# Performance work log

Hardware: AMD Instinct MI355X
Metric: run time of the kernel (lower is better)

## Reference

```python
import jax, jax.numpy as jnp
import numpy as np

# Module dims (match init_kwargs / input_specs)
V = 25        # number of graph nodes (chain skeleton)
K = 3         # max receptive-field size (neighbors incl. self), padded
CIN = 64
COUT = 64
N = 16
T = 512
TK = 3        # temporal_kernel
PAD = TK // 2 # time_pad default


def _build_graph():
    # Chain adjacency with self-links: node i <-> {i-1, i, i+1}
    A = np.zeros((V, V), np.float32)
    for i in range(V):
        A[i, i] = 1.0
        if i > 0:
            A[i, i - 1] = 1.0
        if i < V - 1:
            A[i, i + 1] = 1.0
    # Pad each node's neighbor list to K entries; mask marks real neighbors.
    idx = np.zeros((V, K), np.int32)
    mask = np.zeros((V, K), bool)
    for i in range(V):
        nb = np.where(A[i] != 0)[0]
        idx[i, : len(nb)] = nb
        mask[i, : len(nb)] = True
    return idx, mask


def setup_inputs() -> dict:
    key = jax.random.key(0)
    k_x, k_w, k_b = jax.random.split(key, 3)
    x = jax.random.normal(k_x, (N, CIN, V, T), dtype=jnp.float32)
    # One Conv2d kernel per node: [V, C_out, C_in, K, TK]; padded neighbor
    # slots are zeroed via mask inside reference().
    W = jax.random.normal(k_w, (V, COUT, CIN, K, TK), dtype=jnp.float32) * 0.05
    b = jax.random.normal(k_b, (V, COUT), dtype=jnp.float32) * 0.05
    idx_np, mask_np = _build_graph()
    return {
        "x": x,
        "W": W,
        "b": b,
        "idx": jnp.asarray(idx_np),
        "mask": jnp.asarray(mask_np),
    }


def reference(x, W, b, idx, mask):
    # x: [N, C, V, T]; W: [V, O, C, K, TK]; b: [V, O]; idx/mask: [V, K]
    Tt = x.shape[-1]
    # Zero out padded neighbor slots so padded rows contribute nothing
    # (equivalent to torch's variable-height per-node kernels).
    Wm = jnp.where(mask[:, None, None, :, None], W, 0.0)
    # Temporal zero padding (Conv2d padding=(0, time_pad))
    xp = jnp.pad(x, ((0, 0), (0, 0), (0, 0), (PAD, PAD)))
    # Batched neighbor gather: [N, C, V, K, T + 2*PAD]
    g = xp[:, :, idx, :]
    # Cross-correlation over the TK temporal taps (stride 1)
    out = jnp.zeros((x.shape[0], W.shape[1], V, Tt), dtype=x.dtype)
    for kt in range(TK):
        out = out + jnp.einsum(
            "ncvkt,vock->novt", g[..., kt : kt + Tt], Wm[..., kt]
        )
    out = out + b.T[None, :, :, None]  # per-node bias [O, V]
    return out
```

## Files before the change

kernel.cpp:

```cpp
#include <hip/hip_runtime.h>
#include <hip/hip_bf16.h>

#define NB   16
#define CINC 64
#define COUTC 64
#define NV   25
#define TLEN 512
#define KK   3
#define TKK  3

typedef short short8 __attribute__((ext_vector_type(8)));
typedef float f32x4  __attribute__((ext_vector_type(4)));
typedef float f32x16 __attribute__((ext_vector_type(16)));

#define XT_ROWS 514
#define XS_BYTES 16640
#define NWT3BLK (NV * 9)

__device__ __forceinline__ unsigned pack_bf16(float lo, float hi) {
  __hip_bfloat16 l = __float2bfloat16(lo);
  __hip_bfloat16 h = __float2bfloat16(hi);
  unsigned short ul = *reinterpret_cast<unsigned short*>(&l);
  unsigned short uh = *reinterpret_cast<unsigned short*>(&h);
  return (unsigned)ul | ((unsigned)uh << 16);
}

__global__ __launch_bounds__(256) void prep_all(
    const float* __restrict__ x, const float* __restrict__ W,
    const unsigned char* __restrict__ mask_raw,
    __hip_bfloat16* __restrict__ Wt3, __hip_bfloat16* __restrict__ xT) {
  __shared__ float ts[64][65];
  int bid = blockIdx.x;
  if (bid < NWT3BLK) {
    int blk = bid;
    int v = blk / 9, kkt = blk % 9, k = kkt / 3, kt = kkt % 3;
    const int* mi = (const int*)mask_raw;
    int ok = 1;
    for (int i = 0; i < 18; ++i) {
      int m = mi[i];
      if (m != 0 && m != 1) ok = 0;
    }
    int m = ok ? mi[v * KK + k] : (int)(mask_raw[v * KK + k] != 0);
    const float* Wv = W + (size_t)v * COUTC * CINC * 9;
    __hip_bfloat16* dst = Wt3 + (size_t)blk * 4096;
    for (int i = threadIdx.x; i < 4096; i += 256) {
      int e     = i & 7;
      int lane  = (i >> 3) & 63;
      int ks    = (i >> 9) & 3;
      int oslab = i >> 11;
      int o = oslab * 32 + (lane & 31);
      int c = ks * 16 + 8 * (lane >> 5) + e;
      float val = m ? Wv[(o * CINC + c) * 9 + k * 3 + kt] : 0.f;
      dst[i] = __float2bfloat16(val);
    }
    return;
  }
  bid -= NWT3BLK;
  const int tb = (bid & 7) * 64;
  const int vn = bid >> 3;
  const int v  = vn % NV;
  const int n  = vn / NV;
  const int tid = threadIdx.x;
  for (int i = tid; i < 1024; i += 256) {
    int c = i >> 4, tq = (i & 15) * 4;
    float4 val = *(const float4*)(x + (((size_t)n * CINC + c) * NV + v) * TLEN + tb + tq);
    ts[c][tq + 0] = val.x;
    ts[c][tq + 1] = val.y;
    ts[c][tq + 2] = val.z;
    ts[c][tq + 3] = val.w;
  }
  __syncthreads();
  unsigned* base = (unsigned*)(xT + ((size_t)(n * NV + v) * XT_ROWS) * CINC);
  for (int i = tid; i < 2048; i += 256) {
    int c2 = i & 31, t = i >> 5;
    base[(tb + 1 + t) * 32 + c2] = pack_bf16(ts[2 * c2][t], ts[2 * c2 + 1][t]);
  }
  if (tb == 0 && tid < 32) base[tid] = 0u;
  if (tb == TLEN - 64 && tid < 32) base[513 * 32 + tid] = 0u;
}

__device__ __forceinline__ const char* slab_base(const __hip_bfloat16* xT,
                                                 int n, int vk, int tb) {
  return (const char*)xT + ((size_t)(n * NV + vk) * XT_ROWS + tb) * 128;
}

__global__ __launch_bounds__(256) void lcn_mfma32(
    const __hip_bfloat16* __restrict__ xT,
    const __hip_bfloat16* __restrict__ Wt3,
    const float* __restrict__ bias,
    const int* __restrict__ idx,
    float* __restrict__ out) {
  __shared__ char xs[KK][XS_BYTES];

  const int tb   = blockIdx.x * 128;
  const int n    = blockIdx.y;
  const int v    = blockIdx.z;
  const int tid  = threadIdx.x;
  const int lane = tid & 63;
  const int wave = tid >> 6;
  const int wt   = wave * 32;
  const int hi   = lane >> 5;
  const int l31  = lane & 31;

  {
    const char* g0 = slab_base(xT, n, idx[v * KK + 0], tb);
    const char* g1 = slab_base(xT, n, idx[v * KK + 1], tb);
    const char* g2 = slab_base(xT, n, idx[v * KK + 2], tb);
    for (int j = wave; j < 3 * 17; j += 4) {
      int slab = j / 17, c = j % 17;
      const char* gb = slab == 0 ? g0 : (slab == 1 ? g1 : g2);
      int L = c * 1024 + lane * 16;
      if (L < XS_BYTES) {
        int g = L ^ (((L >> 7) & 7) << 4);
        __builtin_amdgcn_global_load_lds(
            (const __attribute__((address_space(1))) void*)(gb + g),
            (__attribute__((address_space(3))) void*)(&xs[slab][c * 1024]),
            16, 0, 0);
      }
    }
  }
  __syncthreads();

  f32x16 acc0 = {}, acc1 = {};
  const short8* wbase = (const short8*)Wt3;

#pragma unroll
  for (int k = 0; k < KK; ++k) {
    const char* cb = xs[k];
    const int blk0 = (v * KK + k) * TKK;
#pragma unroll
    for (int kt = 0; kt < TKK; ++kt) {
      short8 a0[4], a1[4];
      {
        const short8* p0 = wbase + (((blk0 + kt) * 2 + 0) << 8) + lane;
        const short8* p1 = wbase + (((blk0 + kt) * 2 + 1) << 8) + lane;
#pragma unroll
        for (int ks = 0; ks < 4; ++ks) {
          a0[ks] = p0[ks << 6];
          a1[ks] = p1[ks << 6];
        }
      }
      const int r  = wt + l31 + kt;
      const int sw = (r & 7) << 4;
      const int co = hi * 16;
      const char* bp = cb + r * 128;
#pragma unroll
      for (int ks = 0; ks < 4; ++ks) {
        short8 bfr = *(const short8*)(bp + ((co + 32 * ks) ^ sw));
        acc0 = __builtin_amdgcn_mfma_f32_32x32x16_bf16(a0[ks], bfr, acc0, 0, 0, 0);
        acc1 = __builtin_amdgcn_mfma_f32_32x32x16_bf16(a1[ks], bfr, acc1, 0, 0, 0);
      }
    }
  }

  const float* bv = bias + v * COUTC;
  const int t = tb + wt + l31;
#pragma unroll
  for (int os = 0; os < 2; ++os) {
    const f32x16& acc = os ? acc1 : acc0;
#pragma unroll
    for (int reg = 0; reg < 16; ++reg) {
      int o = os * 32 + 4 * hi + (reg & 3) + 8 * (reg >> 2);
      out[(((size_t)n * COUTC + o) * NV + v) * TLEN + t] = acc[reg] + bv[o];
    }
  }
}

__global__ void prep_mask_kernel(const int* __restrict__ mask_raw,
                                 int* __restrict__ mask_out) {
  __shared__ int fmt;
  if (threadIdx.x == 0) {
    int ok = 1;
    for (int i = 0; i < 18; ++i) {
      int m = mask_raw[i];
      if (m != 0 && m != 1) ok = 0;
    }
    fmt = ok;
  }
  __syncthreads();
  int i = threadIdx.x;
  if (i < NV * KK) {
    int m;
    if (fmt) m = mask_raw[i];
    else     m = (((const unsigned char*)mask_raw)[i] != 0) ? 1 : 0;
    mask_out[i] = m;
  }
}

__global__ void prep_wt_kernel(const float* __restrict__ W,
                               float* __restrict__ Wt) {
  int v   = blockIdx.x / 9;
  int kkt = blockIdx.x % 9;
  const float* Wv = W + (size_t)v * COUTC * CINC * 9;
  float* dst = Wt + (size_t)blockIdx.x * (CINC * COUTC);
  for (int i = threadIdx.x; i < CINC * COUTC; i += 256) {
    int c = i >> 6;
    int o = i & 63;
    dst[i] = Wv[(o * CINC + c) * 9 + kkt];
  }
}

__global__ __launch_bounds__(256, 4) void lcn_main(
    const float* __restrict__ x, const float* __restrict__ Wt,
    const float* __restrict__ b, const int* __restrict__ idx,
    const int* __restrict__ maskn, float* __restrict__ out) {
  __shared__ float xsf[CINC][66];
  __shared__ float wsh[CINC][COUTC];
  const int tb  = blockIdx.x * 64;
  const int v   = blockIdx.y;
  const int n   = blockIdx.z;
  const int tid = threadIdx.x;
  const int t0  = tid & 63;
  const int og  = tid >> 6;
  float acc[16];
#pragma unroll
  for (int j = 0; j < 16; ++j) acc[j] = 0.f;
  for (int k = 0; k < KK; ++k) {
    const int vk = idx[v * KK + k];
    const int mk = maskn[v * KK + k];
    __syncthreads();
    for (int i = tid; i < CINC * 66; i += 256) {
      int c  = i / 66;
      int tt = i - c * 66;
      int gt = tb - 1 + tt;
      float val = 0.f;
      if (mk && gt >= 0 && gt < TLEN)
        val = x[(((size_t)n * CINC + c) * NV + vk) * TLEN + gt];
      xsf[c][tt] = val;
    }
    for (int kt = 0; kt < TKK; ++kt) {
      __syncthreads();
      const float4* src =
          (const float4*)(Wt + ((size_t)(v * KK + k) * TKK + kt) * (CINC * COUTC));
      for (int i = tid; i < CINC * COUTC / 4; i += 256)
        ((float4*)wsh)[i] = src[i];
      __syncthreads();
#pragma unroll 4
      for (int c = 0; c < CINC; ++c) {
        float xv = xsf[c][t0 + kt];
        const float4* wrow = (const float4*)&wsh[c][og * 16];
#pragma unroll
        for (int j4 = 0; j4 < 4; ++j4) {
          float4 wv = wrow[j4];
          acc[j4 * 4 + 0] = fmaf(wv.x, xv, acc[j4 * 4 + 0]);
          acc[j4 * 4 + 1] = fmaf(wv.y, xv, acc[j4 * 4 + 1]);
          acc[j4 * 4 + 2] = fmaf(wv.z, xv, acc[j4 * 4 + 2]);
          acc[j4 * 4 + 3] = fmaf(wv.w, xv, acc[j4 * 4 + 3]);
        }
      }
    }
  }
#pragma unroll
  for (int j = 0; j < 16; ++j) {
    int o = og * 16 + j;
    out[(((size_t)n * COUTC + o) * NV + v) * TLEN + tb + t0] =
        acc[j] + b[v * COUTC + o];
  }
}

extern "C" void kernel_launch(void* const* d_in, const int* in_sizes, int n_in,
                              void* d_out, int out_size, void* d_ws, size_t ws_size,
                              hipStream_t stream) {
  const float* x    = (const float*)d_in[0];
  const float* W    = (const float*)d_in[1];
  const float* b    = (const float*)d_in[2];
  const int*   idx  = (const int*)d_in[3];
  const void*  mask = (const void*)d_in[4];
  float* out = (float*)d_out;

  const size_t WT3_BYTES = (size_t)NV * 9 * 4096 * sizeof(__hip_bfloat16);
  const size_t XT_BYTES  = (size_t)NB * NV * XT_ROWS * CINC * sizeof(__hip_bfloat16);
  const size_t NEED      = 512 + WT3_BYTES + XT_BYTES + 2048;

  if (ws_size >= NEED) {
    __hip_bfloat16* Wt3 = (__hip_bfloat16*)((char*)d_ws + 512);
    __hip_bfloat16* xT  = (__hip_bfloat16*)((char*)d_ws + 512 + WT3_BYTES);
    hipLaunchKernelGGL(prep_all, dim3(NWT3BLK + 8 * NV * NB), dim3(256), 0,
                       stream, x, W, (const unsigned char*)mask, Wt3, xT);
    hipLaunchKernelGGL(lcn_mfma32, dim3(TLEN / 128, NB, NV), dim3(256), 0,
                       stream, xT, Wt3, b, idx, out);
  } else {
    int*   maskn = (int*)d_ws;
    float* Wt    = (float*)((char*)d_ws + 512);
    hipLaunchKernelGGL(prep_mask_kernel, dim3(1), dim3(128), 0, stream,
                       (const int*)mask, maskn);
    hipLaunchKernelGGL(prep_wt_kernel, dim3(NV * KK * TKK), dim3(256), 0, stream,
                       W, Wt);
    hipLaunchKernelGGL(lcn_main, dim3(TLEN / 64, NV, NB), dim3(256), 0, stream,
                       x, Wt, b, idx, maskn, out);
  }
}
```

Before: 54.59 us.

## Repartition waves by output-channel half and preload all weights into registers

```diff
diff --git a/kernel.cpp b/kernel.cpp
--- a/kernel.cpp
+++ b/kernel.cpp
@@ -84,7 +84,7 @@
   return (const char*)xT + ((size_t)(n * NV + vk) * XT_ROWS + tb) * 128;
 }
 
-__global__ __launch_bounds__(256) void lcn_mfma32(
+__global__ __launch_bounds__(256, 2) void lcn_mfma32(
     const __hip_bfloat16* __restrict__ xT,
     const __hip_bfloat16* __restrict__ Wt3,
     const float* __restrict__ bias,
@@ -98,7 +98,8 @@
   const int tid  = threadIdx.x;
   const int lane = tid & 63;
   const int wave = tid >> 6;
-  const int wt   = wave * 32;
+  const int os   = wave & 1;
+  const int th   = wave >> 1;
   const int hi   = lane >> 5;
   const int l31  = lane & 31;
 
@@ -119,45 +120,57 @@
       }
     }
   }
+
+  short8 a[9][4];
+  {
+    const short8* wb = (const short8*)Wt3 + ((size_t)(v * 9) * 2 + os) * 256 + lane;
+#pragma unroll
+    for (int bq = 0; bq < 9; ++bq)
+#pragma unroll
+      for (int ks = 0; ks < 4; ++ks)
+        a[bq][ks] = wb[bq * 512 + (ks << 6)];
+  }
+
   __syncthreads();
 
   f32x16 acc0 = {}, acc1 = {};
-  const short8* wbase = (const short8*)Wt3;
 
 #pragma unroll
   for (int k = 0; k < KK; ++k) {
     const char* cb = xs[k];
-    const int blk0 = (v * KK + k) * TKK;
 #pragma unroll
     for (int kt = 0; kt < TKK; ++kt) {
-      short8 a0[4], a1[4];
+      const int bq = k * TKK + kt;
       {
-        const short8* p0 = wbase + (((blk0 + kt) * 2 + 0) << 8) + lane;
-        const short8* p1 = wbase + (((blk0 + kt) * 2 + 1) << 8) + lane;
+        const int r  = th * 64 + l31 + kt;
+        const int sw = (r & 7) << 4;
+        const int co = hi * 16;
+        const char* bp = cb + r * 128;
 #pragma unroll
         for (int ks = 0; ks < 4; ++ks) {
-          a0[ks] = p0[ks << 6];
-          a1[ks] = p1[ks << 6];
+          short8 bfr = *(const short8*)(bp + ((co + 32 * ks) ^ sw));
+          acc0 = __builtin_amdgcn_mfma_f32_32x32x16_bf16(a[bq][ks], bfr, acc0, 0, 0, 0);
         }
       }
-      const int r  = wt + l31 + kt;
-      const int sw = (r & 7) << 4;
-      const int co = hi * 16;
-      const char* bp = cb + r * 128;
-#pragma unroll
-      for (int ks = 0; ks < 4; ++ks) {
-        short8 bfr = *(const short8*)(bp + ((co + 32 * ks) ^ sw));
-        acc0 = __builtin_amdgcn_mfma_f32_32x32x16_bf16(a0[ks], bfr, acc0, 0, 0, 0);
-        acc1 = __builtin_amdgcn_mfma_f32_32x32x16_bf16(a1[ks], bfr, acc1, 0, 0, 0);
+      {
+        const int r  = th * 64 + 32 + l31 + kt;
+        const int sw = (r & 7) << 4;
+        const int co = hi * 16;
+        const char* bp = cb + r * 128;
+#pragma unroll
+        for (int ks = 0; ks < 4; ++ks) {
+          short8 bfr = *(const short8*)(bp + ((co + 32 * ks) ^ sw));
+          acc1 = __builtin_amdgcn_mfma_f32_32x32x16_bf16(a[bq][ks], bfr, acc1, 0, 0, 0);
+        }
       }
     }
   }
 
   const float* bv = bias + v * COUTC;
-  const int t = tb + wt + l31;
-#pragma unroll
-  for (int os = 0; os < 2; ++os) {
-    const f32x16& acc = os ? acc1 : acc0;
+#pragma unroll
+  for (int s = 0; s < 2; ++s) {
+    const f32x16& acc = s ? acc1 : acc0;
+    const int t = tb + th * 64 + s * 32 + l31;
 #pragma unroll
     for (int reg = 0; reg < 16; ++reg) {
       int o = os * 32 + 4 * hi + (reg & 3) + 8 * (reg >> 2);
```

Result: faster. 50.63 us (-7.3%).
